# Performance work log

Hardware: AMD Instinct MI355X
Metric: run time of the kernel (lower is better)

## Reference

```python
import jax, jax.numpy as jnp
import numpy as np
from jax.ops import segment_sum

N_NODES = 100000
N_EDGES = 1600000

def setup_inputs() -> dict:
    key = jax.random.key(0)
    ks = jax.random.split(key, 16)
    s = 0.1
    return {
        "x": jax.random.normal(ks[0], (N_NODES, 8), jnp.float32),
        "edge_index": jax.random.randint(ks[1], (2, N_EDGES), 0, N_NODES, jnp.int32),
        "W1l": jax.random.normal(ks[2], (8, 128)) * s,
        "W1r": jax.random.normal(ks[3], (8, 128)) * s,
        "b1": jnp.zeros((128,)),
        "W2l": jax.random.normal(ks[4], (128, 128)) * s,
        "W2r": jax.random.normal(ks[5], (128, 128)) * s,
        "b2": jnp.zeros((128,)),
        "W3l": jax.random.normal(ks[6], (128, 1)) * s,
        "W3r": jax.random.normal(ks[7], (128, 1)) * s,
        "b3": jnp.zeros((1,)),
        "Ta1_W": jax.random.normal(ks[8], (4, 8, 8)) * s,
        "Ta1_b": jnp.zeros((8,)),
        "Ta2_W": jax.random.normal(ks[9], (4, 8, 1)) * s,
        "Ta2_b": jnp.zeros((1,)),
        "Tb1_W": jax.random.normal(ks[10], (10, 8, 8)) * s,
        "Tb1_b": jnp.zeros((8,)),
        "Tb2_W": jax.random.normal(ks[11], (10, 8, 1)) * s,
        "Tb2_b": jnp.zeros((1,)),
        "lin2_W": jax.random.normal(ks[12], (2, 1)) * s,
        "lin2_b": jnp.zeros((1,)),
        "lin1_W": jax.random.normal(ks[13], (2, 1)) * s,
        "lin1_b": jnp.zeros((1,)),
    }

def reference(x, edge_index, W1l, W1r, b1, W2l, W2r, b2, W3l, W3r, b3,
              Ta1_W, Ta1_b, Ta2_W, Ta2_b, Tb1_W, Tb1_b, Tb2_W, Tb2_b,
              lin2_W, lin2_b, lin1_W, lin1_b):
    N = x.shape[0]
    src, dst = edge_index[0], edge_index[1]  # message flows src -> dst

    # in-degree of each target node (edge weight = 1)
    deg = segment_sum(jnp.ones_like(src, dtype=x.dtype), dst, num_segments=N)

    # --- SAGEConv: lin_l(mean_{j in N(i)} x_j) + lin_r(x_i) + bias ---
    inv_deg = jnp.where(deg > 0, 1.0 / jnp.maximum(deg, 1.0), 0.0)
    def sage(h, Wl, Wr, b):
        agg = segment_sum(h[src], dst, num_segments=N) * inv_deg[:, None]
        return agg @ Wl + h @ Wr + b

    # --- TAGConv: sym-normalized adjacency powers, no self loops ---
    dinv = jnp.where(deg > 0, jax.lax.rsqrt(jnp.maximum(deg, 1.0)), 0.0)
    norm = dinv[src] * dinv[dst]  # [E]
    def tag(h, Ws, b):  # Ws: [K+1, in, out]
        out = h @ Ws[0]
        for k in range(1, Ws.shape[0]):
            h = segment_sum(h[src] * norm[:, None], dst, num_segments=N)
            out = out + h @ Ws[k]
        return out + b

    relu = jax.nn.relu
    x1 = relu(sage(x, W1l, W1r, b1))
    x1 = relu(sage(x1, W2l, W2r, b2))
    x1 = relu(sage(x1, W3l, W3r, b3))

    x2 = relu(tag(x, Ta1_W, Ta1_b))
    x2 = relu(tag(x2, Ta2_W, Ta2_b))

    x3 = relu(tag(x, Tb1_W, Tb1_b))
    x3 = relu(tag(x3, Tb2_W, Tb2_b))

    x23 = relu(jnp.concatenate([x2, x3], axis=1) @ lin2_W + lin2_b)
    out = relu(jnp.concatenate([x1, x23], axis=1) @ lin1_W + lin1_b)
    return out
```

## Files before the change

kernel.cpp:

```cpp
#include <hip/hip_runtime.h>

#define NN 100000
#define NE 1600000
#define TPB 256

__global__ void k_init(int* __restrict__ deg, int* __restrict__ cursor, int* __restrict__ counter) {
    int i = blockIdx.x * TPB + threadIdx.x;
    if (i < NN) { deg[i] = 0; cursor[i] = 0; }
    if (i == 0) counter[0] = 0;
}

__global__ void k_deg(const int* __restrict__ dst, int* __restrict__ deg) {
    int e = blockIdx.x * TPB + threadIdx.x;
    if (e < NE) atomicAdd(&deg[dst[e]], 1);
}

__global__ void k_prep(const int* __restrict__ deg, float* __restrict__ inv_deg,
                       float* __restrict__ dinv, int* __restrict__ row_start,
                       int* __restrict__ counter) {
    int i = blockIdx.x * TPB + threadIdx.x;
    if (i < NN) {
        int d = deg[i];
        inv_deg[i] = d > 0 ? 1.0f / (float)d : 0.0f;
        dinv[i]    = d > 0 ? 1.0f / sqrtf((float)d) : 0.0f;
        row_start[i] = atomicAdd(counter, d);
    }
}

__global__ void k_fill(const int* __restrict__ src, const int* __restrict__ dst,
                       const int* __restrict__ row_start, int* __restrict__ cursor,
                       int* __restrict__ col) {
    int e = blockIdx.x * TPB + threadIdx.x;
    if (e < NE) {
        int d = dst[e];
        int p = atomicAdd(&cursor[d], 1);
        col[row_start[d] + p] = src[e];
    }
}

__global__ void k_meanprop8(const float* __restrict__ h, const int* __restrict__ row_start,
                            const int* __restrict__ deg, const float* __restrict__ inv_deg,
                            const int* __restrict__ col, float* __restrict__ out) {
    int t = blockIdx.x * TPB + threadIdx.x;
    if (t >= NN * 2) return;
    int n = t >> 1, half = t & 1;
    int rs = row_start[n], end = rs + deg[n];
    const float4* h4 = (const float4*)h;
    float4 s0 = make_float4(0,0,0,0), s1 = make_float4(0,0,0,0);
    int e = rs + half;
    for (; e + 2 < end; e += 4) {
        int c0 = col[e] * 2, c1 = col[e + 2] * 2;
        float4 a0 = h4[c0], a1 = h4[c0 + 1], b0 = h4[c1], b1 = h4[c1 + 1];
        s0.x += a0.x + b0.x; s0.y += a0.y + b0.y; s0.z += a0.z + b0.z; s0.w += a0.w + b0.w;
        s1.x += a1.x + b1.x; s1.y += a1.y + b1.y; s1.z += a1.z + b1.z; s1.w += a1.w + b1.w;
    }
    if (e < end) {
        int c0 = col[e] * 2;
        float4 a0 = h4[c0], a1 = h4[c0 + 1];
        s0.x += a0.x; s0.y += a0.y; s0.z += a0.z; s0.w += a0.w;
        s1.x += a1.x; s1.y += a1.y; s1.z += a1.z; s1.w += a1.w;
    }
    s0.x += __shfl_xor(s0.x, 1, 64); s0.y += __shfl_xor(s0.y, 1, 64);
    s0.z += __shfl_xor(s0.z, 1, 64); s0.w += __shfl_xor(s0.w, 1, 64);
    s1.x += __shfl_xor(s1.x, 1, 64); s1.y += __shfl_xor(s1.y, 1, 64);
    s1.z += __shfl_xor(s1.z, 1, 64); s1.w += __shfl_xor(s1.w, 1, 64);
    float w = inv_deg[n];
    float4 o = (half == 0) ? s0 : s1;
    o.x *= w; o.y *= w; o.z *= w; o.w *= w;
    ((float4*)out)[n * 2 + half] = o;
}

__global__ void k_meanprop128(const float* __restrict__ h, const int* __restrict__ row_start,
                              const int* __restrict__ deg, const float* __restrict__ inv_deg,
                              const int* __restrict__ col, float* __restrict__ out) {
    int t = blockIdx.x * TPB + threadIdx.x;
    if (t >= NN * 32) return;
    int n = t >> 5, f4 = t & 31;
    int rs = row_start[n], d = deg[n];
    const float4* h4 = (const float4*)h;
    float4 s = make_float4(0.f, 0.f, 0.f, 0.f);
    for (int e = rs; e < rs + d; ++e) {
        int c = col[e];
        float4 v = h4[(size_t)c * 32 + f4];
        s.x += v.x; s.y += v.y; s.z += v.z; s.w += v.w;
    }
    float w = inv_deg[n];
    s.x *= w; s.y *= w; s.z *= w; s.w *= w;
    ((float4*)out)[t] = s;
}

__global__ void k_tagstep(const float* __restrict__ q, const int* __restrict__ row_start,
                          const int* __restrict__ deg, const float* __restrict__ dinv,
                          const int* __restrict__ col, float* __restrict__ qout,
                          const float* __restrict__ Wa, const float* __restrict__ Wb,
                          float* __restrict__ outa, float* __restrict__ outb,
                          const float* __restrict__ ba, const float* __restrict__ bb,
                          int fina, int finb) {
    int t = blockIdx.x * TPB + threadIdx.x;
    if (t >= NN * 2) return;
    int n = t >> 1, half = t & 1;
    int rs = row_start[n], end = rs + deg[n];
    const float4* q4 = (const float4*)q;
    float4 s0 = make_float4(0,0,0,0), s1 = make_float4(0,0,0,0);
    int e = rs + half;
    for (; e + 2 < end; e += 4) {
        int c0 = col[e] * 2, c1 = col[e + 2] * 2;
        float4 a0 = q4[c0], a1 = q4[c0 + 1], b0 = q4[c1], b1 = q4[c1 + 1];
        s0.x += a0.x + b0.x; s0.y += a0.y + b0.y; s0.z += a0.z + b0.z; s0.w += a0.w + b0.w;
        s1.x += a1.x + b1.x; s1.y += a1.y + b1.y; s1.z += a1.z + b1.z; s1.w += a1.w + b1.w;
    }
    if (e < end) {
        int c0 = col[e] * 2;
        float4 a0 = q4[c0], a1 = q4[c0 + 1];
        s0.x += a0.x; s0.y += a0.y; s0.z += a0.z; s0.w += a0.w;
        s1.x += a1.x; s1.y += a1.y; s1.z += a1.z; s1.w += a1.w;
    }
    s0.x += __shfl_xor(s0.x, 1, 64); s0.y += __shfl_xor(s0.y, 1, 64);
    s0.z += __shfl_xor(s0.z, 1, 64); s0.w += __shfl_xor(s0.w, 1, 64);
    s1.x += __shfl_xor(s1.x, 1, 64); s1.y += __shfl_xor(s1.y, 1, 64);
    s1.z += __shfl_xor(s1.z, 1, 64); s1.w += __shfl_xor(s1.w, 1, 64);
    float dn = dinv[n];
    float h[8] = { s0.x * dn, s0.y * dn, s0.z * dn, s0.w * dn,
                   s1.x * dn, s1.y * dn, s1.z * dn, s1.w * dn };
    int f0 = half * 4;
    if (qout) {
        float4 qv = make_float4(h[f0] * dn, h[f0 + 1] * dn, h[f0 + 2] * dn, h[f0 + 3] * dn);
        ((float4*)qout)[n * 2 + half] = qv;
    }
    if (Wa) {
        float4 o = ((float4*)outa)[n * 2 + half];
        float av[4] = { o.x, o.y, o.z, o.w };
        #pragma unroll
        for (int j = 0; j < 8; ++j) {
            float hv = h[j];
            #pragma unroll
            for (int f = 0; f < 4; ++f) av[f] += hv * Wa[j * 8 + f0 + f];
        }
        if (fina) {
            #pragma unroll
            for (int f = 0; f < 4; ++f) av[f] = fmaxf(av[f] + ba[f0 + f], 0.f);
        }
        ((float4*)outa)[n * 2 + half] = make_float4(av[0], av[1], av[2], av[3]);
    }
    {
        float4 o = ((float4*)outb)[n * 2 + half];
        float bv[4] = { o.x, o.y, o.z, o.w };
        #pragma unroll
        for (int j = 0; j < 8; ++j) {
            float hv = h[j];
            #pragma unroll
            for (int f = 0; f < 4; ++f) bv[f] += hv * Wb[j * 8 + f0 + f];
        }
        if (finb) {
            #pragma unroll
            for (int f = 0; f < 4; ++f) bv[f] = fmaxf(bv[f] + bb[f0 + f], 0.f);
        }
        ((float4*)outb)[n * 2 + half] = make_float4(bv[0], bv[1], bv[2], bv[3]);
    }
}

__global__ void k_symprop1n(const float* __restrict__ qin, const float* __restrict__ yk,
                            const int* __restrict__ row_start, const int* __restrict__ deg,
                            const float* __restrict__ dinv, const int* __restrict__ col,
                            float* __restrict__ qout, int qstride,
                            float* __restrict__ fout, const float* __restrict__ bias) {
    int t = blockIdx.x * TPB + threadIdx.x;
    if (t >= NN * 4) return;
    int n = t >> 2, qd = t & 3;
    int rs = row_start[n], d = deg[n];
    float s = 0.f;
    for (int e = rs + qd; e < rs + d; e += 4) s += qin[col[e]];
    s += __shfl_xor(s, 1, 64);
    s += __shfl_xor(s, 2, 64);
    if (qd == 0) {
        float dn = dinv[n];
        float v = dn * s + yk[n];
        if (fout) fout[n] = fmaxf(v + bias[0], 0.f);
        else      qout[(size_t)n * qstride] = dn * v;
    }
}

__global__ void k_symprop2(const float* __restrict__ q2in, const float* __restrict__ yka,
                           const float* __restrict__ ykb, const int* __restrict__ row_start,
                           const int* __restrict__ deg, const float* __restrict__ dinv,
                           const int* __restrict__ col, float* __restrict__ q2out,
                           float* __restrict__ fa, float* __restrict__ fb,
                           const float* __restrict__ biasa, const float* __restrict__ biasb) {
    int t = blockIdx.x * TPB + threadIdx.x;
    if (t >= NN * 4) return;
    int n = t >> 2, qd = t & 3;
    int rs = row_start[n], d = deg[n];
    const float2* q2 = (const float2*)q2in;
    float sa = 0.f, sb = 0.f;
    for (int e = rs + qd; e < rs + d; e += 4) {
        float2 v = q2[col[e]];
        sa += v.x; sb += v.y;
    }
    sa += __shfl_xor(sa, 1, 64); sa += __shfl_xor(sa, 2, 64);
    sb += __shfl_xor(sb, 1, 64); sb += __shfl_xor(sb, 2, 64);
    if (qd == 0) {
        float dn = dinv[n];
        float va = dn * sa + yka[n];
        float vb = dn * sb + ykb[n];
        if (fa) {
            fa[n] = fmaxf(va + biasa[0], 0.f);
            fb[n] = fmaxf(vb + biasb[0], 0.f);
        } else {
            ((float2*)q2out)[n] = make_float2(dn * va, dn * vb);
        }
    }
}

__global__ void k_sage3(const float* __restrict__ yl, const float* __restrict__ yr,
                        const int* __restrict__ row_start, const int* __restrict__ deg,
                        const float* __restrict__ inv_deg, const int* __restrict__ col,
                        const float* __restrict__ b3, float* __restrict__ x1f) {
    int t = blockIdx.x * TPB + threadIdx.x;
    if (t >= NN * 4) return;
    int n = t >> 2, q = t & 3;
    int rs = row_start[n], d = deg[n];
    float s = 0.f;
    for (int e = rs + q; e < rs + d; e += 4) s += yl[col[e]];
    s += __shfl_xor(s, 1, 64);
    s += __shfl_xor(s, 2, 64);
    if (q == 0) x1f[n] = fmaxf(s * inv_deg[n] + yr[n] + b3[0], 0.f);
}

__global__ void k_sage1(const float* __restrict__ a8, const float* __restrict__ x,
                        const float* __restrict__ W1l, const float* __restrict__ W1r,
                        const float* __restrict__ b1, float* __restrict__ x1) {
    int t = blockIdx.x * TPB + threadIdx.x;
    if (t >= NN * 16) return;
    int n = t >> 4, og = (t & 15) * 8;
    float acc[8];
    #pragma unroll
    for (int j = 0; j < 8; ++j) acc[j] = b1[og + j];
    const float* ar = a8 + (size_t)n * 8;
    const float* xr = x + (size_t)n * 8;
    #pragma unroll
    for (int k = 0; k < 8; ++k) {
        float av = ar[k], xv = xr[k];
        const float4* wl = (const float4*)(W1l + k * 128 + og);
        const float4* wr = (const float4*)(W1r + k * 128 + og);
        float4 l0 = wl[0], l1 = wl[1], r0 = wr[0], r1 = wr[1];
        acc[0] += av * l0.x + xv * r0.x;
        acc[1] += av * l0.y + xv * r0.y;
        acc[2] += av * l0.z + xv * r0.z;
        acc[3] += av * l0.w + xv * r0.w;
        acc[4] += av * l1.x + xv * r1.x;
        acc[5] += av * l1.y + xv * r1.y;
        acc[6] += av * l1.z + xv * r1.z;
        acc[7] += av * l1.w + xv * r1.w;
    }
    #pragma unroll
    for (int j = 0; j < 8; ++j)
        x1[(size_t)n * 128 + og + j] = fmaxf(acc[j], 0.f);
}

__global__ __launch_bounds__(256) void k_transpose(const float* __restrict__ in0,
        float* __restrict__ out0, const float* __restrict__ in1, float* __restrict__ out1) {
    const float* in = blockIdx.y ? in1 : in0;
    float* outp = blockIdx.y ? out1 : out0;
    __shared__ float t[128][65];
    int n0 = blockIdx.x * 64;
    int tid = threadIdx.x;
    #pragma unroll
    for (int i = 0; i < 8; ++i) {
        int idx = tid + i * 256;
        int nl = idx >> 5;
        int kq = (idx & 31) << 2;
        int n = n0 + nl;
        float4 v = (n < NN) ? *(const float4*)(in + (size_t)n * 128 + kq)
                            : make_float4(0.f, 0.f, 0.f, 0.f);
        t[kq][nl] = v.x; t[kq + 1][nl] = v.y; t[kq + 2][nl] = v.z; t[kq + 3][nl] = v.w;
    }
    __syncthreads();
    #pragma unroll
    for (int i = 0; i < 8; ++i) {
        int idx = tid + i * 256;
        int k = idx >> 4;
        int nq = (idx & 15) << 2;
        if (n0 + nq + 3 < NN) {
            float4 v = make_float4(t[k][nq], t[k][nq + 1], t[k][nq + 2], t[k][nq + 3]);
            *(float4*)(outp + (size_t)k * NN + n0 + nq) = v;
        }
    }
}

__global__ __launch_bounds__(256) void k_sage2t(const float* __restrict__ aT,
        const float* __restrict__ xT, const float* __restrict__ W2l,
        const float* __restrict__ W2r, const float* __restrict__ b2,
        float* __restrict__ oT) {
    int n0 = blockIdx.x * 256 + threadIdx.x;
    int n = (n0 < NN) ? n0 : (NN - 1);
    int og = blockIdx.y * 32;
    float acc[32];
    #pragma unroll
    for (int j = 0; j < 32; ++j) acc[j] = b2[og + j];
    const float* ap = aT + n;
    const float* xp = xT + n;
    const float* wlp = W2l + og;
    const float* wrp = W2r + og;
    #pragma unroll 2
    for (int k = 0; k < 128; ++k) {
        float a = ap[0], xv = xp[0];
        ap += NN; xp += NN;
        const float4* wl4 = (const float4*)(wlp + (k << 7));
        const float4* wr4 = (const float4*)(wrp + (k << 7));
        #pragma unroll
        for (int q = 0; q < 8; ++q) {
            float4 wl = wl4[q], wr = wr4[q];
            acc[q * 4 + 0] += a * wl.x + xv * wr.x;
            acc[q * 4 + 1] += a * wl.y + xv * wr.y;
            acc[q * 4 + 2] += a * wl.z + xv * wr.z;
            acc[q * 4 + 3] += a * wl.w + xv * wr.w;
        }
    }
    if (n0 < NN) {
        float* op = oT + (size_t)og * NN + n0;
        #pragma unroll
        for (int j = 0; j < 32; ++j) {
            op[0] = fmaxf(acc[j], 0.f);
            op += NN;
        }
    }
}

__global__ void k_dotsT(const float* __restrict__ oT, const float* __restrict__ W3l,
                        const float* __restrict__ W3r, float* __restrict__ yl,
                        float* __restrict__ yr) {
    int n = blockIdx.x * TPB + threadIdx.x;
    if (n >= NN) return;
    const float* p = oT + n;
    float pl = 0.f, pr = 0.f;
    #pragma unroll 4
    for (int k = 0; k < 128; ++k) {
        float v = p[0];
        p += NN;
        pl += v * W3l[k];
        pr += v * W3r[k];
    }
    yl[n] = pl;
    yr[n] = pr;
}

__global__ void k_taginit(const float* __restrict__ x, const float* __restrict__ TaW,
                          const float* __restrict__ TbW, const float* __restrict__ dinv,
                          float* __restrict__ outa, float* __restrict__ outb,
                          float* __restrict__ q0) {
    int t = blockIdx.x * TPB + threadIdx.x;
    if (t >= NN * 8) return;
    int n = t >> 3, o = t & 7;
    const float* xr = x + (size_t)n * 8;
    float sa = 0.f, sb = 0.f;
    #pragma unroll
    for (int j = 0; j < 8; ++j) {
        float v = xr[j];
        sa += v * TaW[j * 8 + o];
        sb += v * TbW[j * 8 + o];
    }
    outa[t] = sa;
    outb[t] = sb;
    q0[t] = xr[o] * dinv[n];
}

__global__ void k_tag2proj(const float* __restrict__ h8, const float* __restrict__ W,
                           float* __restrict__ y, int K1, const float* __restrict__ dinv,
                           float* __restrict__ qlast, int qstride) {
    int n = blockIdx.x * TPB + threadIdx.x;
    if (n >= NN) return;
    float hr[8];
    #pragma unroll
    for (int j = 0; j < 8; ++j) hr[j] = h8[(size_t)n * 8 + j];
    for (int k = 0; k < K1; ++k) {
        float s = 0.f;
        #pragma unroll
        for (int j = 0; j < 8; ++j) s += hr[j] * W[k * 8 + j];
        if (k == K1 - 1) qlast[(size_t)n * qstride] = s * dinv[n];
        else             y[(size_t)k * NN + n] = s;
    }
}

__global__ void k_final(const float* __restrict__ x1f, const float* __restrict__ x2s,
                        const float* __restrict__ x3s, const float* __restrict__ l2w,
                        const float* __restrict__ l2b, const float* __restrict__ l1w,
                        const float* __restrict__ l1b, float* __restrict__ out) {
    int n = blockIdx.x * TPB + threadIdx.x;
    if (n >= NN) return;
    float x23 = fmaxf(x2s[n] * l2w[0] + x3s[n] * l2w[1] + l2b[0], 0.f);
    out[n] = fmaxf(x1f[n] * l1w[0] + x23 * l1w[1] + l1b[0], 0.f);
}

#define GL(kern, n, ...) \
    kern<<<dim3((unsigned)(((long)(n) + TPB - 1) / TPB)), dim3(TPB), 0, stream>>>(__VA_ARGS__)

extern "C" void kernel_launch(void* const* d_in, const int* in_sizes, int n_in,
                              void* d_out, int out_size, void* d_ws, size_t ws_size,
                              hipStream_t stream) {
    (void)in_sizes; (void)n_in; (void)out_size; (void)ws_size;
    const float* x   = (const float*)d_in[0];
    const int*   ei  = (const int*)d_in[1];
    const int*   src = ei;
    const int*   dst = ei + NE;
    const float* W1l = (const float*)d_in[2];
    const float* W1r = (const float*)d_in[3];
    const float* b1  = (const float*)d_in[4];
    const float* W2l = (const float*)d_in[5];
    const float* W2r = (const float*)d_in[6];
    const float* b2  = (const float*)d_in[7];
    const float* W3l = (const float*)d_in[8];
    const float* W3r = (const float*)d_in[9];
    const float* b3  = (const float*)d_in[10];
    const float* TaW1 = (const float*)d_in[11];
    const float* TaB1 = (const float*)d_in[12];
    const float* TaW2 = (const float*)d_in[13];
    const float* TaB2 = (const float*)d_in[14];
    const float* TbW1 = (const float*)d_in[15];
    const float* TbB1 = (const float*)d_in[16];
    const float* TbW2 = (const float*)d_in[17];
    const float* TbB2 = (const float*)d_in[18];
    const float* l2w = (const float*)d_in[19];
    const float* l2b = (const float*)d_in[20];
    const float* l1w = (const float*)d_in[21];
    const float* l1b = (const float*)d_in[22];
    float* out = (float*)d_out;

    char* p = (char*)d_ws;
    size_t off = 0;
    auto alloc = [&](size_t bytes) -> void* {
        void* r = p + off;
        off = (off + bytes + 255) & ~(size_t)255;
        return r;
    };
    int*   deg       = (int*)  alloc((size_t)NN * 4);
    float* inv_deg   = (float*)alloc((size_t)NN * 4);
    float* dinv      = (float*)alloc((size_t)NN * 4);
    int*   row_start = (int*)  alloc((size_t)NN * 4);
    int*   cursor    = (int*)  alloc((size_t)NN * 4);
    int*   counter   = (int*)  alloc(256);
    int*   col       = (int*)  alloc((size_t)NE * 4);
    float* a8        = (float*)alloc((size_t)NN * 8 * 4);
    float* qA        = (float*)alloc((size_t)NN * 8 * 4);
    float* qB        = (float*)alloc((size_t)NN * 8 * 4);
    float* outa      = (float*)alloc((size_t)NN * 8 * 4);
    float* outb      = (float*)alloc((size_t)NN * 8 * 4);
    float* x1        = (float*)alloc((size_t)NN * 128 * 4);
    float* a128      = (float*)alloc((size_t)NN * 128 * 4);
    float* a128T     = (float*)alloc((size_t)NN * 128 * 4);
    float* x1T       = (float*)alloc((size_t)NN * 128 * 4);
    float* yl        = (float*)alloc((size_t)NN * 4);
    float* yr        = (float*)alloc((size_t)NN * 4);
    float* x1f       = (float*)alloc((size_t)NN * 4);
    float* x2s       = (float*)alloc((size_t)NN * 4);
    float* x3s       = (float*)alloc((size_t)NN * 4);
    float* tA        = (float*)alloc((size_t)NN * 4);
    float* tB        = (float*)alloc((size_t)NN * 4);
    float* qb0       = (float*)alloc((size_t)NN * 4);
    float* q2a       = (float*)alloc((size_t)NN * 8);
    float* q2b       = (float*)alloc((size_t)NN * 8);
    float* ya        = (float*)alloc((size_t)NN * 4 * 4);
    float* yb        = (float*)alloc((size_t)NN * 10 * 4);
    float* x1bT      = a128;

    GL(k_init, NN, deg, cursor, counter);
    GL(k_deg, NE, dst, deg);
    GL(k_prep, NN, deg, inv_deg, dinv, row_start, counter);
    GL(k_fill, NE, src, dst, row_start, cursor, col);

    GL(k_meanprop8, (long)NN * 2, x, row_start, deg, inv_deg, col, a8);
    GL(k_sage1, (long)NN * 16, a8, x, W1l, W1r, b1, x1);
    GL(k_meanprop128, (long)NN * 32, x1, row_start, deg, inv_deg, col, a128);
    k_transpose<<<dim3((NN + 63) / 64, 2), dim3(256), 0, stream>>>(a128, a128T, x1, x1T);
    k_sage2t<<<dim3((NN + 255) / 256, 4), dim3(256), 0, stream>>>(a128T, x1T, W2l, W2r, b2, x1bT);
    GL(k_dotsT, NN, x1bT, W3l, W3r, yl, yr);
    GL(k_sage3, (long)NN * 4, yl, yr, row_start, deg, inv_deg, col, b3, x1f);

    GL(k_taginit, (long)NN * 8, x, TaW1, TbW1, dinv, outa, outb, qA);
    {
        float* qcur = qA;
        float* qnext = qB;
        for (int k = 1; k <= 9; ++k) {
            float* qout = (k < 9) ? qnext : nullptr;
            const float* Wa = (k <= 3) ? (TaW1 + (size_t)k * 64) : nullptr;
            GL(k_tagstep, (long)NN * 2, qcur, row_start, deg, dinv, col, qout,
               Wa, TbW1 + (size_t)k * 64, outa, outb, TaB1, TbB1,
               (k == 3) ? 1 : 0, (k == 9) ? 1 : 0);
            if (qout) { float* tmp = qcur; qcur = qnext; qnext = tmp; }
        }
    }

    GL(k_tag2proj, NN, outa, TaW2, ya, 4, dinv, q2a, 2);
    GL(k_tag2proj, NN, outb, TbW2, yb, 10, dinv, qb0, 1);

    GL(k_symprop1n, (long)NN * 4, qb0, yb + 8 * NN, row_start, deg, dinv, col, tA, 1, (float*)nullptr, (const float*)nullptr);
    GL(k_symprop1n, (long)NN * 4, tA,  yb + 7 * NN, row_start, deg, dinv, col, tB, 1, (float*)nullptr, (const float*)nullptr);
    GL(k_symprop1n, (long)NN * 4, tB,  yb + 6 * NN, row_start, deg, dinv, col, tA, 1, (float*)nullptr, (const float*)nullptr);
    GL(k_symprop1n, (long)NN * 4, tA,  yb + 5 * NN, row_start, deg, dinv, col, tB, 1, (float*)nullptr, (const float*)nullptr);
    GL(k_symprop1n, (long)NN * 4, tB,  yb + 4 * NN, row_start, deg, dinv, col, tA, 1, (float*)nullptr, (const float*)nullptr);
    GL(k_symprop1n, (long)NN * 4, tA,  yb + 3 * NN, row_start, deg, dinv, col, q2a + 1, 2, (float*)nullptr, (const float*)nullptr);

    GL(k_symprop2, (long)NN * 4, q2a, ya + 2 * NN, yb + 2 * NN, row_start, deg, dinv, col, q2b,
       (float*)nullptr, (float*)nullptr, (const float*)nullptr, (const float*)nullptr);
    GL(k_symprop2, (long)NN * 4, q2b, ya + 1 * NN, yb + 1 * NN, row_start, deg, dinv, col, q2a,
       (float*)nullptr, (float*)nullptr, (const float*)nullptr, (const float*)nullptr);
    GL(k_symprop2, (long)NN * 4, q2a, ya + 0 * NN, yb + 0 * NN, row_start, deg, dinv, col, (float*)nullptr,
       x2s, x3s, TaB2, TbB2);

    GL(k_final, NN, x1f, x2s, x3s, l2w, l2b, l1w, l1b, out);
}
```

Baseline: 854.2 us.

## Fuse SAGE layer-3 projection into layer-2 GEMM and merge tail kernels

The layer-2 SAGE kernel now computes 64 outputs per thread and immediately applies ReLU and dot-products with W3l/W3r, writing two partial scalars per node. This removes the 128xN intermediate write and the separate k_dotsT reread. The two TAG projection kernels are merged into one, and the final linear layers are folded into the last symmetric propagation kernel, dropping launches and intermediate buffers. The wider 64-element accumulator raises register pressure and halves the grid in y, which may lower occupancy.

```diff
diff --git a/kernel.cpp b/kernel.cpp
--- a/kernel.cpp
+++ b/kernel.cpp
@@ -162,8 +162,7 @@
 __global__ void k_symprop1n(const float* __restrict__ qin, const float* __restrict__ yk,
                             const int* __restrict__ row_start, const int* __restrict__ deg,
                             const float* __restrict__ dinv, const int* __restrict__ col,
-                            float* __restrict__ qout, int qstride,
-                            float* __restrict__ fout, const float* __restrict__ bias) {
+                            float* __restrict__ qout, int qstride) {
     int t = blockIdx.x * TPB + threadIdx.x;
     if (t >= NN * 4) return;
     int n = t >> 2, qd = t & 3;
@@ -174,18 +173,14 @@
     s += __shfl_xor(s, 2, 64);
     if (qd == 0) {
         float dn = dinv[n];
-        float v = dn * s + yk[n];
-        if (fout) fout[n] = fmaxf(v + bias[0], 0.f);
-        else      qout[(size_t)n * qstride] = dn * v;
+        qout[(size_t)n * qstride] = dn * (dn * s + yk[n]);
     }
 }
 
 __global__ void k_symprop2(const float* __restrict__ q2in, const float* __restrict__ yka,
                            const float* __restrict__ ykb, const int* __restrict__ row_start,
                            const int* __restrict__ deg, const float* __restrict__ dinv,
-                           const int* __restrict__ col, float* __restrict__ q2out,
-                           float* __restrict__ fa, float* __restrict__ fb,
-                           const float* __restrict__ biasa, const float* __restrict__ biasb) {
+                           const int* __restrict__ col, float* __restrict__ q2out) {
     int t = blockIdx.x * TPB + threadIdx.x;
     if (t >= NN * 4) return;
     int n = t >> 2, qd = t & 3;
@@ -200,18 +195,42 @@
     sb += __shfl_xor(sb, 1, 64); sb += __shfl_xor(sb, 2, 64);
     if (qd == 0) {
         float dn = dinv[n];
-        float va = dn * sa + yka[n];
-        float vb = dn * sb + ykb[n];
-        if (fa) {
-            fa[n] = fmaxf(va + biasa[0], 0.f);
-            fb[n] = fmaxf(vb + biasb[0], 0.f);
-        } else {
-            ((float2*)q2out)[n] = make_float2(dn * va, dn * vb);
-        }
-    }
-}
-
-__global__ void k_sage3(const float* __restrict__ yl, const float* __restrict__ yr,
+        ((float2*)q2out)[n] = make_float2(dn * (dn * sa + yka[n]),
+                                          dn * (dn * sb + ykb[n]));
+    }
+}
+
+__global__ void k_symprop2fin(const float* __restrict__ q2in, const float* __restrict__ yka,
+                              const float* __restrict__ ykb, const int* __restrict__ row_start,
+                              const int* __restrict__ deg, const float* __restrict__ dinv,
+                              const int* __restrict__ col,
+                              const float* __restrict__ biasa, const float* __restrict__ biasb,
+                              const float* __restrict__ x1f,
+                              const float* __restrict__ l2w, const float* __restrict__ l2b,
+                              const float* __restrict__ l1w, const float* __restrict__ l1b,
+                              float* __restrict__ out) {
+    int t = blockIdx.x * TPB + threadIdx.x;
+    if (t >= NN * 4) return;
+    int n = t >> 2, qd = t & 3;
+    int rs = row_start[n], d = deg[n];
+    const float2* q2 = (const float2*)q2in;
+    float sa = 0.f, sb = 0.f;
+    for (int e = rs + qd; e < rs + d; e += 4) {
+        float2 v = q2[col[e]];
+        sa += v.x; sb += v.y;
+    }
+    sa += __shfl_xor(sa, 1, 64); sa += __shfl_xor(sa, 2, 64);
+    sb += __shfl_xor(sb, 1, 64); sb += __shfl_xor(sb, 2, 64);
+    if (qd == 0) {
+        float dn = dinv[n];
+        float x2 = fmaxf(dn * sa + yka[n] + biasa[0], 0.f);
+        float x3 = fmaxf(dn * sb + ykb[n] + biasb[0], 0.f);
+        float x23 = fmaxf(x2 * l2w[0] + x3 * l2w[1] + l2b[0], 0.f);
+        out[n] = fmaxf(x1f[n] * l1w[0] + x23 * l1w[1] + l1b[0], 0.f);
+    }
+}
+
+__global__ void k_sage3(const float* __restrict__ ylp, const float* __restrict__ yrp,
                         const int* __restrict__ row_start, const int* __restrict__ deg,
                         const float* __restrict__ inv_deg, const int* __restrict__ col,
                         const float* __restrict__ b3, float* __restrict__ x1f) {
@@ -220,10 +239,16 @@
     int n = t >> 2, q = t & 3;
     int rs = row_start[n], d = deg[n];
     float s = 0.f;
-    for (int e = rs + q; e < rs + d; e += 4) s += yl[col[e]];
+    for (int e = rs + q; e < rs + d; e += 4) {
+        int c = col[e];
+        s += ylp[c] + ylp[NN + c];
+    }
     s += __shfl_xor(s, 1, 64);
     s += __shfl_xor(s, 2, 64);
-    if (q == 0) x1f[n] = fmaxf(s * inv_deg[n] + yr[n] + b3[0], 0.f);
+    if (q == 0) {
+        float yr = yrp[n] + yrp[NN + n];
+        x1f[n] = fmaxf(s * inv_deg[n] + yr + b3[0], 0.f);
+    }
 }
 
 __global__ void k_sage1(const float* __restrict__ a8, const float* __restrict__ x,
@@ -287,16 +312,17 @@
     }
 }
 
-__global__ __launch_bounds__(256) void k_sage2t(const float* __restrict__ aT,
+__global__ __launch_bounds__(256) void k_sage2f(const float* __restrict__ aT,
         const float* __restrict__ xT, const float* __restrict__ W2l,
         const float* __restrict__ W2r, const float* __restrict__ b2,
-        float* __restrict__ oT) {
+        const float* __restrict__ W3l, const float* __restrict__ W3r,
+        float* __restrict__ ylp, float* __restrict__ yrp) {
     int n0 = blockIdx.x * 256 + threadIdx.x;
     int n = (n0 < NN) ? n0 : (NN - 1);
-    int og = blockIdx.y * 32;
-    float acc[32];
-    #pragma unroll
-    for (int j = 0; j < 32; ++j) acc[j] = b2[og + j];
+    int og = blockIdx.y * 64;
+    float acc[64];
+    #pragma unroll
+    for (int j = 0; j < 64; ++j) acc[j] = b2[og + j];
     const float* ap = aT + n;
     const float* xp = xT + n;
     const float* wlp = W2l + og;
@@ -308,7 +334,7 @@
         const float4* wl4 = (const float4*)(wlp + (k << 7));
         const float4* wr4 = (const float4*)(wrp + (k << 7));
         #pragma unroll
-        for (int q = 0; q < 8; ++q) {
+        for (int q = 0; q < 16; ++q) {
             float4 wl = wl4[q], wr = wr4[q];
             acc[q * 4 + 0] += a * wl.x + xv * wr.x;
             acc[q * 4 + 1] += a * wl.y + xv * wr.y;
@@ -316,32 +342,17 @@
             acc[q * 4 + 3] += a * wl.w + xv * wr.w;
         }
     }
+    float pl = 0.f, pr = 0.f;
+    #pragma unroll
+    for (int j = 0; j < 64; ++j) {
+        float v = fmaxf(acc[j], 0.f);
+        pl += v * W3l[og + j];
+        pr += v * W3r[og + j];
+    }
     if (n0 < NN) {
-        float* op = oT + (size_t)og * NN + n0;
-        #pragma unroll
-        for (int j = 0; j < 32; ++j) {
-            op[0] = fmaxf(acc[j], 0.f);
-            op += NN;
-        }
-    }
-}
-
-__global__ void k_dotsT(const float* __restrict__ oT, const float* __restrict__ W3l,
-                        const float* __restrict__ W3r, float* __restrict__ yl,
-                        float* __restrict__ yr) {
-    int n = blockIdx.x * TPB + threadIdx.x;
-    if (n >= NN) return;
-    const float* p = oT + n;
-    float pl = 0.f, pr = 0.f;
-    #pragma unroll 4
-    for (int k = 0; k < 128; ++k) {
-        float v = p[0];
-        p += NN;
-        pl += v * W3l[k];
-        pr += v * W3r[k];
-    }
-    yl[n] = pl;
-    yr[n] = pr;
+        ylp[(size_t)blockIdx.y * NN + n0] = pl;
+        yrp[(size_t)blockIdx.y * NN + n0] = pr;
+    }
 }
 
 __global__ void k_taginit(const float* __restrict__ x, const float* __restrict__ TaW,
@@ -364,31 +375,35 @@
     q0[t] = xr[o] * dinv[n];
 }
 
-__global__ void k_tag2proj(const float* __restrict__ h8, const float* __restrict__ W,
-                           float* __restrict__ y, int K1, const float* __restrict__ dinv,
-                           float* __restrict__ qlast, int qstride) {
+__global__ void k_tag2projAB(const float* __restrict__ outa, const float* __restrict__ outb,
+                             const float* __restrict__ TaW2, const float* __restrict__ TbW2,
+                             float* __restrict__ ya, float* __restrict__ yb,
+                             const float* __restrict__ dinv,
+                             float* __restrict__ q2a, float* __restrict__ qb0) {
     int n = blockIdx.x * TPB + threadIdx.x;
     if (n >= NN) return;
-    float hr[8];
-    #pragma unroll
-    for (int j = 0; j < 8; ++j) hr[j] = h8[(size_t)n * 8 + j];
-    for (int k = 0; k < K1; ++k) {
+    float dn = dinv[n];
+    float ha[8], hb[8];
+    #pragma unroll
+    for (int j = 0; j < 8; ++j) ha[j] = outa[(size_t)n * 8 + j];
+    #pragma unroll
+    for (int j = 0; j < 8; ++j) hb[j] = outb[(size_t)n * 8 + j];
+    #pragma unroll
+    for (int k = 0; k < 4; ++k) {
         float s = 0.f;
         #pragma unroll
-        for (int j = 0; j < 8; ++j) s += hr[j] * W[k * 8 + j];
-        if (k == K1 - 1) qlast[(size_t)n * qstride] = s * dinv[n];
-        else             y[(size_t)k * NN + n] = s;
-    }
-}
-
-__global__ void k_final(const float* __restrict__ x1f, const float* __restrict__ x2s,
-                        const float* __restrict__ x3s, const float* __restrict__ l2w,
-                        const float* __restrict__ l2b, const float* __restrict__ l1w,
-                        const float* __restrict__ l1b, float* __restrict__ out) {
-    int n = blockIdx.x * TPB + threadIdx.x;
-    if (n >= NN) return;
-    float x23 = fmaxf(x2s[n] * l2w[0] + x3s[n] * l2w[1] + l2b[0], 0.f);
-    out[n] = fmaxf(x1f[n] * l1w[0] + x23 * l1w[1] + l1b[0], 0.f);
+        for (int j = 0; j < 8; ++j) s += ha[j] * TaW2[k * 8 + j];
+        if (k == 3) q2a[(size_t)n * 2] = s * dn;
+        else        ya[(size_t)k * NN + n] = s;
+    }
+    #pragma unroll
+    for (int k = 0; k < 10; ++k) {
+        float s = 0.f;
+        #pragma unroll
+        for (int j = 0; j < 8; ++j) s += hb[j] * TbW2[k * 8 + j];
+        if (k == 9) qb0[n] = s * dn;
+        else        yb[(size_t)k * NN + n] = s;
+    }
 }
 
 #define GL(kern, n, ...) \
@@ -448,11 +463,9 @@
     float* a128      = (float*)alloc((size_t)NN * 128 * 4);
     float* a128T     = (float*)alloc((size_t)NN * 128 * 4);
     float* x1T       = (float*)alloc((size_t)NN * 128 * 4);
-    float* yl        = (float*)alloc((size_t)NN * 4);
-    float* yr        = (float*)alloc((size_t)NN * 4);
+    float* ylp       = (float*)alloc((size_t)NN * 2 * 4);
+    float* yrp       = (float*)alloc((size_t)NN * 2 * 4);
     float* x1f       = (float*)alloc((size_t)NN * 4);
-    float* x2s       = (float*)alloc((size_t)NN * 4);
-    float* x3s       = (float*)alloc((size_t)NN * 4);
     float* tA        = (float*)alloc((size_t)NN * 4);
     float* tB        = (float*)alloc((size_t)NN * 4);
     float* qb0       = (float*)alloc((size_t)NN * 4);
@@ -460,7 +473,6 @@
     float* q2b       = (float*)alloc((size_t)NN * 8);
     float* ya        = (float*)alloc((size_t)NN * 4 * 4);
     float* yb        = (float*)alloc((size_t)NN * 10 * 4);
-    float* x1bT      = a128;
 
     GL(k_init, NN, deg, cursor, counter);
     GL(k_deg, NE, dst, deg);
@@ -471,9 +483,8 @@
     GL(k_sage1, (long)NN * 16, a8, x, W1l, W1r, b1, x1);
     GL(k_meanprop128, (long)NN * 32, x1, row_start, deg, inv_deg, col, a128);
     k_transpose<<<dim3((NN + 63) / 64, 2), dim3(256), 0, stream>>>(a128, a128T, x1, x1T);
-    k_sage2t<<<dim3((NN + 255) / 256, 4), dim3(256), 0, stream>>>(a128T, x1T, W2l, W2r, b2, x1bT);
-    GL(k_dotsT, NN, x1bT, W3l, W3r, yl, yr);
-    GL(k_sage3, (long)NN * 4, yl, yr, row_start, deg, inv_deg, col, b3, x1f);
+    k_sage2f<<<dim3((NN + 255) / 256, 2), dim3(256), 0, stream>>>(a128T, x1T, W2l, W2r, b2, W3l, W3r, ylp, yrp);
+    GL(k_sage3, (long)NN * 4, ylp, yrp, row_start, deg, inv_deg, col, b3, x1f);
 
     GL(k_taginit, (long)NN * 8, x, TaW1, TbW1, dinv, outa, outb, qA);
     {
@@ -489,22 +500,17 @@
         }
     }
 
-    GL(k_tag2proj, NN, outa, TaW2, ya, 4, dinv, q2a, 2);
-    GL(k_tag2proj, NN, outb, TbW2, yb, 10, dinv, qb0, 1);
-
-    GL(k_symprop1n, (long)NN * 4, qb0, yb + 8 * NN, row_start, deg, dinv, col, tA, 1, (float*)nullptr, (const float*)nullptr);
-    GL(k_symprop1n, (long)NN * 4, tA,  yb + 7 * NN, row_start, deg, dinv, col, tB, 1, (float*)nullptr, (const float*)nullptr);
-    GL(k_symprop1n, (long)NN * 4, tB,  yb + 6 * NN, row_start, deg, dinv, col, tA, 1, (float*)nullptr, (const float*)nullptr);
-    GL(k_symprop1n, (long)NN * 4, tA,  yb + 5 * NN, row_start, deg, dinv, col, tB, 1, (float*)nullptr, (const float*)nullptr);
-    GL(k_symprop1n, (long)NN * 4, tB,  yb + 4 * NN, row_start, deg, dinv, col, tA, 1, (float*)nullptr, (const float*)nullptr);
-    GL(k_symprop1n, (long)NN * 4, tA,  yb + 3 * NN, row_start, deg, dinv, col, q2a + 1, 2, (float*)nullptr, (const float*)nullptr);
-
-    GL(k_symprop2, (long)NN * 4, q2a, ya + 2 * NN, yb + 2 * NN, row_start, deg, dinv, col, q2b,
-       (float*)nullptr, (float*)nullptr, (const float*)nullptr, (const float*)nullptr);
-    GL(k_symprop2, (long)NN * 4, q2b, ya + 1 * NN, yb + 1 * NN, row_start, deg, dinv, col, q2a,
-       (float*)nullptr, (float*)nullptr, (const float*)nullptr, (const float*)nullptr);
-    GL(k_symprop2, (long)NN * 4, q2a, ya + 0 * NN, yb + 0 * NN, row_start, deg, dinv, col, (float*)nullptr,
-       x2s, x3s, TaB2, TbB2);
-
-    GL(k_final, NN, x1f, x2s, x3s, l2w, l2b, l1w, l1b, out);
-}
+    GL(k_tag2projAB, NN, outa, outb, TaW2, TbW2, ya, yb, dinv, q2a, qb0);
+
+    GL(k_symprop1n, (long)NN * 4, qb0, yb + 8 * NN, row_start, deg, dinv, col, tA, 1);
+    GL(k_symprop1n, (long)NN * 4, tA,  yb + 7 * NN, row_start, deg, dinv, col, tB, 1);
+    GL(k_symprop1n, (long)NN * 4, tB,  yb + 6 * NN, row_start, deg, dinv, col, tA, 1);
+    GL(k_symprop1n, (long)NN * 4, tA,  yb + 5 * NN, row_start, deg, dinv, col, tB, 1);
+    GL(k_symprop1n, (long)NN * 4, tB,  yb + 4 * NN, row_start, deg, dinv, col, tA, 1);
+    GL(k_symprop1n, (long)NN * 4, tA,  yb + 3 * NN, row_start, deg, dinv, col, q2a + 1, 2);
+
+    GL(k_symprop2, (long)NN * 4, q2a, ya + 2 * NN, yb + 2 * NN, row_start, deg, dinv, col, q2b);
+    GL(k_symprop2, (long)NN * 4, q2b, ya + 1 * NN, yb + 1 * NN, row_start, deg, dinv, col, q2a);
+    GL(k_symprop2fin, (long)NN * 4, q2a, ya + 0 * NN, yb + 0 * NN, row_start, deg, dinv, col,
+       TaB2, TbB2, x1f, l2w, l2b, l1w, l1b, out);
+}
```

Measured after the change: 861.8 us. Within noise of the previous version (+0.9%).
